# Optimization experiments

Hardware: AMD Instinct MI355X
Metric: run time of the kernel (lower is better)

The kernel has to match this reference:

```python
import jax, jax.numpy as jnp
import numpy as np

FP4_E2M1_VALUES = [0.0, 0.0625, 8.0, 1.0, 2.0, 3.0, 4.0, 6.0,
                   -0.0, -0.0625, -8.0, -1.0, -2.0, -3.0, -4.0, -6.0]

M, N, K = 4096, 4096, 4096


def setup_inputs() -> dict:
    key = jax.random.key(0)
    k1, k2 = jax.random.split(key)
    x = jax.random.normal(k1, (M, K), dtype=jnp.float16)
    # packed uint8 bytes stored as int32 (values in [0,256)); each byte holds
    # two fp4 indices: high nibble = even k, low nibble = odd k
    packed_weight = jax.random.randint(k2, (N, K // 2), 0, 256, dtype=jnp.int32)
    lut = jnp.array(FP4_E2M1_VALUES, dtype=jnp.float16)
    return {"x": x, "packed_weight": packed_weight, "lut": lut}


def reference(x, packed_weight, lut):
    # Dequantize: unpack nibbles along K, LUT lookup -> W [N, K] fp16
    n, kh = packed_weight.shape
    high = (packed_weight >> 4) & 15   # even k positions
    low = packed_weight & 15           # odd k positions
    idx = jnp.stack([high, low], axis=-1).reshape(n, 2 * kh)  # [N, K]
    w = lut[idx]                       # [N, K] fp16
    # GEMM with fp32 accumulation (Triton kernel accumulates in fp32), cast to fp16
    y = jnp.einsum('mk,nk->mn', x, w, preferred_element_type=jnp.float32)
    return y.astype(jnp.float16)
```

## Files before the change

### kernel.cpp

```cpp
#include <hip/hip_runtime.h>
#include <hip/hip_fp16.h>
#include <stdint.h>

#define M_DIM 4096
#define N_DIM 4096
#define K_DIM 4096
#define KW (K_DIM / 2)
#define WS_XH_BYTES ((size_t)M_DIM * K_DIM * 2)
#define WS_WH_BYTES ((size_t)N_DIM * K_DIM * 2)

typedef _Float16 half8 __attribute__((ext_vector_type(8)));
typedef float f32x4 __attribute__((ext_vector_type(4)));

__device__ __forceinline__ uint32_t pk2(float a, float b) {
  auto h = __builtin_amdgcn_cvt_pkrtz(a, b);
  return __builtin_bit_cast(uint32_t, h);
}

__device__ __forceinline__ uint32_t dq(uint32_t b, uint32_t ph, uint32_t pl) {
#if __has_builtin(__builtin_amdgcn_perm)
  const uint32_t sel = ((b & 0x70u) << 4) | ((b & 0x07u) << 24);
  uint32_t v = __builtin_amdgcn_perm(ph, pl, sel);
#else
  const uint64_t pool = ((uint64_t)ph << 32) | pl;
  const uint32_t mh = (uint32_t)(pool >> (((b >> 4) & 7u) * 8)) & 0xFFu;
  const uint32_t ml = (uint32_t)(pool >> ((b & 7u) * 8)) & 0xFFu;
  uint32_t v = (mh << 8) | (ml << 24);
#endif
  const uint32_t sg = ((b & 0x88u) * 0x10000100u) & 0x80008000u;
  return v | sg;
}

__device__ __forceinline__ void lut_pool(const float* __restrict__ lutf,
                                         uint32_t& ph, uint32_t& pl) {
  const uint32_t h01 = pk2(lutf[0], lutf[1]);
  const uint32_t h23 = pk2(lutf[2], lutf[3]);
  const uint32_t h45 = pk2(lutf[4], lutf[5]);
  const uint32_t h67 = pk2(lutf[6], lutf[7]);
#if __has_builtin(__builtin_amdgcn_perm)
  pl = __builtin_amdgcn_perm(h23, h01, 0x07050301u);
  ph = __builtin_amdgcn_perm(h67, h45, 0x07050301u);
#else
  pl = ((h01 >> 8) & 0xFFu) | ((h01 >> 24) << 8) |
       (((h23 >> 8) & 0xFFu) << 16) | ((h23 >> 24) << 24);
  ph = ((h45 >> 8) & 0xFFu) | ((h45 >> 24) << 8) |
       (((h67 >> 8) & 0xFFu) << 16) | ((h67 >> 24) << 24);
#endif
}

__global__ __launch_bounds__(256) void cvt_x_kernel(const float4* __restrict__ xin,
                                                    uint4* __restrict__ xout) {
  const int i = blockIdx.x * 256 + threadIdx.x;
  const float4 v0 = xin[2 * i];
  const float4 v1 = xin[2 * i + 1];
  xout[i] = make_uint4(pk2(v0.x, v0.y), pk2(v0.z, v0.w),
                       pk2(v1.x, v1.y), pk2(v1.z, v1.w));
}

__global__ __launch_bounds__(256) void wdq_kernel(const int4* __restrict__ pin,
                                                  uint4* __restrict__ wout,
                                                  const float* __restrict__ lutf) {
  uint32_t ph, pl;
  lut_pool(lutf, ph, pl);
  const int i = blockIdx.x * 256 + threadIdx.x;
  const int4 w = pin[i];
  wout[i] = make_uint4(dq(w.x, ph, pl), dq(w.y, ph, pl),
                       dq(w.z, ph, pl), dq(w.w, ph, pl));
}

__device__ __forceinline__ f32x4 mfma16(half8 a, half8 b, f32x4 c) {
  return __builtin_amdgcn_mfma_f32_16x16x32_f16(a, b, c, 0, 0, 0);
}

#define NT (K_DIM / 64)

__global__ __launch_bounds__(512, 2) void f16gemm256_kernel(
    const uint8_t* __restrict__ xh,
    const uint8_t* __restrict__ wh,
    float* __restrict__ out)
{
  __shared__ uint16_t Al[2][2][256 * 32];
  __shared__ uint16_t Bl[2][2][256 * 32];

  const int tid  = threadIdx.x;
  const int lane = tid & 63;
  const int wave = tid >> 6;
  const int wm   = wave >> 2;
  const int wn   = wave & 3;

  const int bid = blockIdx.x;
  const int sw  = (bid & 7) * 32 + (bid >> 3);
  const int m0  = (sw >> 4) * 256;
  const int n0  = (sw & 15) * 256;

  const uint8_t* asrc[2];
  const uint8_t* bsrc[2];
  int ldst[2];
#pragma unroll
  for (int s = 0; s < 2; ++s) {
    const int slot = tid + s * 512;
    const int row  = slot >> 2;
    const int g    = (slot & 3) ^ ((row >> 1) & 3);
    asrc[s] = xh + ((size_t)(m0 + row) * K_DIM) * 2 + g * 16;
    bsrc[s] = wh + ((size_t)(n0 + row) * K_DIM) * 2 + g * 16;
    ldst[s] = slot * 16;
  }

  auto STAGE = [&](int isB, int buf, int kh, int tt) {
    const int koff  = tt * 128 + kh * 64;
    uint8_t* lb = (uint8_t*)(isB ? &Bl[0][0][0] : &Al[0][0][0]) +
                  (buf * 2 + kh) * 16384;
#pragma unroll
    for (int s = 0; s < 2; ++s) {
      const uint8_t* gp = (isB ? bsrc[s] : asrc[s]) + koff;
      __builtin_amdgcn_global_load_lds(
          (const __attribute__((address_space(1))) uint32_t*)gp,
          (__attribute__((address_space(3))) uint32_t*)(lb + ldst[s]), 16, 0, 0);
    }
  };

  int aoff[8], boff[4];
#pragma unroll
  for (int m = 0; m < 8; ++m) {
    const int row = wm * 128 + m * 16 + (lane & 15);
    const int ch  = (lane >> 4) ^ ((row >> 1) & 3);
    aoff[m] = row * 32 + ch * 8;
  }
#pragma unroll
  for (int n = 0; n < 4; ++n) {
    const int row = wn * 64 + n * 16 + (lane & 15);
    const int ch  = (lane >> 4) ^ ((row >> 1) & 3);
    boff[n] = row * 32 + ch * 8;
  }

  f32x4 acc[8][4];
#pragma unroll
  for (int i = 0; i < 8; ++i)
#pragma unroll
    for (int j = 0; j < 4; ++j) acc[i][j] = (f32x4){0.f, 0.f, 0.f, 0.f};

  STAGE(1, 0, 0, 0);
  STAGE(0, 0, 0, 0);
  STAGE(1, 0, 1, 0);
  STAGE(0, 0, 1, 0);
  STAGE(1, 1, 0, 1);
  STAGE(0, 1, 0, 1);
  asm volatile("s_waitcnt vmcnt(8)" ::: "memory");
  __builtin_amdgcn_s_barrier();

  half8 af[4], bfr[4];

#pragma unroll 2
  for (int t = 0; t < NT; ++t) {
    const int cur = t & 1;
    const uint16_t* Ab = &Al[cur][0][0];
    const uint16_t* Bb = &Bl[cur][0][0];
    const bool st1 = (t + 1 < NT);
    const bool st2 = (t + 2 < NT);

#pragma unroll
    for (int n = 0; n < 4; ++n) bfr[n] = *(const half8*)(Bb + boff[n]);
#pragma unroll
    for (int m = 0; m < 4; ++m) af[m] = *(const half8*)(Ab + aoff[m]);
    if (st1) STAGE(1, cur ^ 1, 1, t + 1);
    __builtin_amdgcn_s_barrier();
    asm volatile("s_waitcnt lgkmcnt(0)" ::: "memory");
    __builtin_amdgcn_sched_barrier(0);
    __builtin_amdgcn_s_setprio(1);
#pragma unroll
    for (int m = 0; m < 4; ++m)
#pragma unroll
      for (int n = 0; n < 4; ++n)
        acc[m][n] = mfma16(af[m], bfr[n], acc[m][n]);
    __builtin_amdgcn_s_setprio(0);
    __builtin_amdgcn_s_barrier();

#pragma unroll
    for (int m = 0; m < 4; ++m) af[m] = *(const half8*)(Ab + aoff[4 + m]);
    if (st1) STAGE(0, cur ^ 1, 1, t + 1);
    __builtin_amdgcn_s_barrier();
    asm volatile("s_waitcnt lgkmcnt(0)" ::: "memory");
    __builtin_amdgcn_sched_barrier(0);
    __builtin_amdgcn_s_setprio(1);
#pragma unroll
    for (int m = 0; m < 4; ++m)
#pragma unroll
      for (int n = 0; n < 4; ++n)
        acc[4 + m][n] = mfma16(af[m], bfr[n], acc[4 + m][n]);
    __builtin_amdgcn_s_setprio(0);
    if (st1) asm volatile("s_waitcnt vmcnt(8)" ::: "memory");
    else     asm volatile("s_waitcnt vmcnt(0)" ::: "memory");
    __builtin_amdgcn_s_barrier();

#pragma unroll
    for (int n = 0; n < 4; ++n) bfr[n] = *(const half8*)(Bb + 8192 + boff[n]);
#pragma unroll
    for (int m = 0; m < 4; ++m) af[m] = *(const half8*)(Ab + 8192 + aoff[m]);
    if (st2) STAGE(1, cur, 0, t + 2);
    __builtin_amdgcn_s_barrier();
    asm volatile("s_waitcnt lgkmcnt(0)" ::: "memory");
    __builtin_amdgcn_sched_barrier(0);
    __builtin_amdgcn_s_setprio(1);
#pragma unroll
    for (int m = 0; m < 4; ++m)
#pragma unroll
      for (int n = 0; n < 4; ++n)
        acc[m][n] = mfma16(af[m], bfr[n], acc[m][n]);
    __builtin_amdgcn_s_setprio(0);
    __builtin_amdgcn_s_barrier();

#pragma unroll
    for (int m = 0; m < 4; ++m) af[m] = *(const half8*)(Ab + 8192 + aoff[4 + m]);
    if (st2) STAGE(0, cur, 0, t + 2);
    __builtin_amdgcn_s_barrier();
    asm volatile("s_waitcnt lgkmcnt(0)" ::: "memory");
    __builtin_amdgcn_sched_barrier(0);
    __builtin_amdgcn_s_setprio(1);
#pragma unroll
    for (int m = 0; m < 4; ++m)
#pragma unroll
      for (int n = 0; n < 4; ++n)
        acc[4 + m][n] = mfma16(af[m], bfr[n], acc[4 + m][n]);
    __builtin_amdgcn_s_setprio(0);
    if (st2)      asm volatile("s_waitcnt vmcnt(8)" ::: "memory");
    else if (st1) asm volatile("s_waitcnt vmcnt(4)" ::: "memory");
    __builtin_amdgcn_s_barrier();
  }

  const int mb = m0 + wm * 128 + (lane >> 4) * 4;
  const int nb = n0 + wn * 64 + (lane & 15);
#pragma unroll
  for (int m = 0; m < 8; ++m)
#pragma unroll
    for (int n = 0; n < 4; ++n)
#pragma unroll
      for (int r = 0; r < 4; ++r)
        out[(size_t)(mb + m * 16 + r) * N_DIM + (nb + n * 16)] = acc[m][n][r];
}

#define BM 128
#define BN 128
#define BK 32

__global__ __launch_bounds__(256, 2) void fp4gemm_kernel(
    const uint8_t* __restrict__ xh, const int* __restrict__ pw,
    const float* __restrict__ lutf, float* __restrict__ out)
{
  __shared__ uint16_t ldsA[BM * BK];
  __shared__ uint16_t ldsB[BN * BK];

  const int tid  = threadIdx.x;
  const int lane = tid & 63;
  const int wave = tid >> 6;
  const int wm   = wave >> 1;
  const int wn   = wave & 1;
  const int m0 = blockIdx.y * BM;
  const int n0 = blockIdx.x * BN;

  uint32_t ph, pl;
  lut_pool(lutf, ph, pl);

  f32x4 acc[4][4];
#pragma unroll
  for (int i = 0; i < 4; ++i)
#pragma unroll
    for (int j = 0; j < 4; ++j) acc[i][j] = (f32x4){0.f, 0.f, 0.f, 0.f};

  const int rowB  = tid >> 1;
  const int halfB = tid & 1;
  const int swzB  = (rowB >> 1) & 3;

  for (int kt = 0; kt < K_DIM / BK; ++kt) {
    __syncthreads();

#pragma unroll
    for (int s = 0; s < 2; ++s) {
      const int idx = tid + s * 256;
      const int row = idx >> 2;
      const int c16 = idx & 3;
      const int g16 = c16 ^ ((row >> 1) & 3);
      const uint8_t* gp = xh + ((size_t)(m0 + row) * K_DIM + kt * BK) * 2 + g16 * 16;
      uint8_t* lp = (uint8_t*)ldsA + (size_t)idx * 16;
      __builtin_amdgcn_global_load_lds(
          (const __attribute__((address_space(1))) uint32_t*)gp,
          (__attribute__((address_space(3))) uint32_t*)lp, 16, 0, 0);
    }

    {
      const int* gp = pw + (size_t)(n0 + rowB) * KW + kt * (BK / 2) + halfB * 8;
      const int4 wA = ((const int4*)gp)[0];
      const int4 wB = ((const int4*)gp)[1];
      uint8_t* base = (uint8_t*)ldsB + rowB * 64;
      *(uint4*)(base + ((halfB * 2 + 0) ^ swzB) * 16) =
          make_uint4(dq(wA.x, ph, pl), dq(wA.y, ph, pl),
                     dq(wA.z, ph, pl), dq(wA.w, ph, pl));
      *(uint4*)(base + ((halfB * 2 + 1) ^ swzB) * 16) =
          make_uint4(dq(wB.x, ph, pl), dq(wB.y, ph, pl),
                     dq(wB.z, ph, pl), dq(wB.w, ph, pl));
    }

    __syncthreads();

    const int q = lane >> 4;
    half8 af[4], bfr[4];
#pragma unroll
    for (int i = 0; i < 4; ++i) {
      const int row = wm * 64 + i * 16 + (lane & 15);
      af[i] = *(const half8*)(ldsA + row * BK + (q ^ ((row >> 1) & 3)) * 8);
    }
#pragma unroll
    for (int j = 0; j < 4; ++j) {
      const int row = wn * 64 + j * 16 + (lane & 15);
      bfr[j] = *(const half8*)(ldsB + row * BK + (q ^ ((row >> 1) & 3)) * 8);
    }
#pragma unroll
    for (int i = 0; i < 4; ++i)
#pragma unroll
      for (int j = 0; j < 4; ++j)
        acc[i][j] = __builtin_amdgcn_mfma_f32_16x16x32_f16(af[i], bfr[j], acc[i][j], 0, 0, 0);
  }

  const int mb = m0 + wm * 64 + (lane >> 4) * 4;
  const int nb = n0 + wn * 64 + (lane & 15);
#pragma unroll
  for (int i = 0; i < 4; ++i)
#pragma unroll
    for (int j = 0; j < 4; ++j)
#pragma unroll
      for (int r = 0; r < 4; ++r)
        out[(size_t)(mb + i * 16 + r) * N_DIM + (nb + j * 16)] = acc[i][j][r];
}

extern "C" void kernel_launch(void* const* d_in, const int* in_sizes, int n_in,
                              void* d_out, int out_size, void* d_ws, size_t ws_size,
                              hipStream_t stream) {
  const void* px = nullptr; const void* ppw = nullptr; const void* plut = nullptr;
  for (int i = 0; i < n_in; ++i) {
    const long s = in_sizes[i];
    if (s == (long)M_DIM * K_DIM) px = d_in[i];
    else if (s == (long)N_DIM * KW) ppw = d_in[i];
    else if (s == 16) plut = d_in[i];
  }
  if (!px || !ppw || !plut) { px = d_in[0]; ppw = d_in[1]; plut = d_in[2]; }

  cvt_x_kernel<<<(M_DIM * K_DIM / 8) / 256, 256, 0, stream>>>(
      (const float4*)px, (uint4*)d_ws);

  if (ws_size >= WS_XH_BYTES + WS_WH_BYTES) {
    uint8_t* wh = (uint8_t*)d_ws + WS_XH_BYTES;
    wdq_kernel<<<(N_DIM * KW / 4) / 256, 256, 0, stream>>>(
        (const int4*)ppw, (uint4*)wh, (const float*)plut);
    f16gemm256_kernel<<<dim3(256), dim3(512), 0, stream>>>(
        (const uint8_t*)d_ws, wh, (float*)d_out);
  } else {
    dim3 grid(N_DIM / BN, M_DIM / BM);
    fp4gemm_kernel<<<grid, dim3(256), 0, stream>>>(
        (const uint8_t*)d_ws, (const int*)ppw, (const float*)plut, (float*)d_out);
  }
}
```

Measured before the change: 268.9 us.

## Fuse prep kernels and collapse GEMM loop into two phases per tile

```diff
diff --git a/kernel.cpp b/kernel.cpp
--- a/kernel.cpp
+++ b/kernel.cpp
@@ -48,6 +48,30 @@
 #endif
 }
 
+#define XBLOCKS (M_DIM * K_DIM / 8 / 256)
+#define WBLOCKS (N_DIM * KW / 4 / 256)
+
+__global__ __launch_bounds__(256) void prep_kernel(
+    const float4* __restrict__ xin, uint4* __restrict__ xout,
+    const int4* __restrict__ pin, uint4* __restrict__ wout,
+    const float* __restrict__ lutf) {
+  const int b = blockIdx.x;
+  if (b < XBLOCKS) {
+    const int i = b * 256 + threadIdx.x;
+    const float4 v0 = xin[2 * i];
+    const float4 v1 = xin[2 * i + 1];
+    xout[i] = make_uint4(pk2(v0.x, v0.y), pk2(v0.z, v0.w),
+                         pk2(v1.x, v1.y), pk2(v1.z, v1.w));
+  } else {
+    uint32_t ph, pl;
+    lut_pool(lutf, ph, pl);
+    const int i = (b - XBLOCKS) * 256 + threadIdx.x;
+    const int4 w = pin[i];
+    wout[i] = make_uint4(dq(w.x, ph, pl), dq(w.y, ph, pl),
+                         dq(w.z, ph, pl), dq(w.w, ph, pl));
+  }
+}
+
 __global__ __launch_bounds__(256) void cvt_x_kernel(const float4* __restrict__ xin,
                                                     uint4* __restrict__ xout) {
   const int i = blockIdx.x * 256 + threadIdx.x;
@@ -55,17 +79,6 @@
   const float4 v1 = xin[2 * i + 1];
   xout[i] = make_uint4(pk2(v0.x, v0.y), pk2(v0.z, v0.w),
                        pk2(v1.x, v1.y), pk2(v1.z, v1.w));
-}
-
-__global__ __launch_bounds__(256) void wdq_kernel(const int4* __restrict__ pin,
-                                                  uint4* __restrict__ wout,
-                                                  const float* __restrict__ lutf) {
-  uint32_t ph, pl;
-  lut_pool(lutf, ph, pl);
-  const int i = blockIdx.x * 256 + threadIdx.x;
-  const int4 w = pin[i];
-  wout[i] = make_uint4(dq(w.x, ph, pl), dq(w.y, ph, pl),
-                       dq(w.z, ph, pl), dq(w.w, ph, pl));
 }
 
 __device__ __forceinline__ f32x4 mfma16(half8 a, half8 b, f32x4 c) {
@@ -148,7 +161,7 @@
   asm volatile("s_waitcnt vmcnt(8)" ::: "memory");
   __builtin_amdgcn_s_barrier();
 
-  half8 af[4], bfr[4];
+  half8 af[8], bfr[4];
 
 #pragma unroll 2
   for (int t = 0; t < NT; ++t) {
@@ -161,32 +174,15 @@
 #pragma unroll
     for (int n = 0; n < 4; ++n) bfr[n] = *(const half8*)(Bb + boff[n]);
 #pragma unroll
-    for (int m = 0; m < 4; ++m) af[m] = *(const half8*)(Ab + aoff[m]);
-    if (st1) STAGE(1, cur ^ 1, 1, t + 1);
+    for (int m = 0; m < 8; ++m) af[m] = *(const half8*)(Ab + aoff[m]);
+    if (st1) { STAGE(1, cur ^ 1, 1, t + 1); STAGE(0, cur ^ 1, 1, t + 1); }
     __builtin_amdgcn_s_barrier();
-    asm volatile("s_waitcnt lgkmcnt(0)" ::: "memory");
-    __builtin_amdgcn_sched_barrier(0);
     __builtin_amdgcn_s_setprio(1);
 #pragma unroll
-    for (int m = 0; m < 4; ++m)
+    for (int m = 0; m < 8; ++m)
 #pragma unroll
       for (int n = 0; n < 4; ++n)
         acc[m][n] = mfma16(af[m], bfr[n], acc[m][n]);
-    __builtin_amdgcn_s_setprio(0);
-    __builtin_amdgcn_s_barrier();
-
-#pragma unroll
-    for (int m = 0; m < 4; ++m) af[m] = *(const half8*)(Ab + aoff[4 + m]);
-    if (st1) STAGE(0, cur ^ 1, 1, t + 1);
-    __builtin_amdgcn_s_barrier();
-    asm volatile("s_waitcnt lgkmcnt(0)" ::: "memory");
-    __builtin_amdgcn_sched_barrier(0);
-    __builtin_amdgcn_s_setprio(1);
-#pragma unroll
-    for (int m = 0; m < 4; ++m)
-#pragma unroll
-      for (int n = 0; n < 4; ++n)
-        acc[4 + m][n] = mfma16(af[m], bfr[n], acc[4 + m][n]);
     __builtin_amdgcn_s_setprio(0);
     if (st1) asm volatile("s_waitcnt vmcnt(8)" ::: "memory");
     else     asm volatile("s_waitcnt vmcnt(0)" ::: "memory");
@@ -195,32 +191,15 @@
 #pragma unroll
     for (int n = 0; n < 4; ++n) bfr[n] = *(const half8*)(Bb + 8192 + boff[n]);
 #pragma unroll
-    for (int m = 0; m < 4; ++m) af[m] = *(const half8*)(Ab + 8192 + aoff[m]);
-    if (st2) STAGE(1, cur, 0, t + 2);
+    for (int m = 0; m < 8; ++m) af[m] = *(const half8*)(Ab + 8192 + aoff[m]);
+    if (st2) { STAGE(1, cur, 0, t + 2); STAGE(0, cur, 0, t + 2); }
     __builtin_amdgcn_s_barrier();
-    asm volatile("s_waitcnt lgkmcnt(0)" ::: "memory");
-    __builtin_amdgcn_sched_barrier(0);
     __builtin_amdgcn_s_setprio(1);
 #pragma unroll
-    for (int m = 0; m < 4; ++m)
+    for (int m = 0; m < 8; ++m)
 #pragma unroll
       for (int n = 0; n < 4; ++n)
         acc[m][n] = mfma16(af[m], bfr[n], acc[m][n]);
-    __builtin_amdgcn_s_setprio(0);
-    __builtin_amdgcn_s_barrier();
-
-#pragma unroll
-    for (int m = 0; m < 4; ++m) af[m] = *(const half8*)(Ab + 8192 + aoff[4 + m]);
-    if (st2) STAGE(0, cur, 0, t + 2);
-    __builtin_amdgcn_s_barrier();
-    asm volatile("s_waitcnt lgkmcnt(0)" ::: "memory");
-    __builtin_amdgcn_sched_barrier(0);
-    __builtin_amdgcn_s_setprio(1);
-#pragma unroll
-    for (int m = 0; m < 4; ++m)
-#pragma unroll
-      for (int n = 0; n < 4; ++n)
-        acc[4 + m][n] = mfma16(af[m], bfr[n], acc[4 + m][n]);
     __builtin_amdgcn_s_setprio(0);
     if (st2)      asm volatile("s_waitcnt vmcnt(8)" ::: "memory");
     else if (st1) asm volatile("s_waitcnt vmcnt(4)" ::: "memory");
@@ -343,16 +322,16 @@
   }
   if (!px || !ppw || !plut) { px = d_in[0]; ppw = d_in[1]; plut = d_in[2]; }
 
-  cvt_x_kernel<<<(M_DIM * K_DIM / 8) / 256, 256, 0, stream>>>(
-      (const float4*)px, (uint4*)d_ws);
-
   if (ws_size >= WS_XH_BYTES + WS_WH_BYTES) {
     uint8_t* wh = (uint8_t*)d_ws + WS_XH_BYTES;
-    wdq_kernel<<<(N_DIM * KW / 4) / 256, 256, 0, stream>>>(
-        (const int4*)ppw, (uint4*)wh, (const float*)plut);
+    prep_kernel<<<XBLOCKS + WBLOCKS, 256, 0, stream>>>(
+        (const float4*)px, (uint4*)d_ws, (const int4*)ppw, (uint4*)wh,
+        (const float*)plut);
     f16gemm256_kernel<<<dim3(256), dim3(512), 0, stream>>>(
         (const uint8_t*)d_ws, wh, (float*)d_out);
   } else {
+    cvt_x_kernel<<<(M_DIM * K_DIM / 8) / 256, 256, 0, stream>>>(
+        (const float4*)px, (uint4*)d_ws);
     dim3 grid(N_DIM / BN, M_DIM / BM);
     fp4gemm_kernel<<<grid, dim3(256), 0, stream>>>(
         (const uint8_t*)d_ws, (const int*)ppw, (const float*)plut, (float*)d_out);
```

Result: no change. 265.7 us (-1.2%).
